# Kernel tuning notes

Hardware: AMD Instinct MI355X
Metric: run time of the kernel (lower is better)

The kernel has to match this reference:

```python
import jax, jax.numpy as jnp
import numpy as np

D_MODEL = 1024
NUM_HEADS = 16
HEAD_DIM = D_MODEL // NUM_HEADS
BATCH = 2
SEQ = 2048


def setup_inputs() -> dict:
    key = jax.random.key(0)
    ks = jax.random.split(key, 9)
    s = 1.0 / np.sqrt(D_MODEL)
    inp = {
        "x": jax.random.normal(ks[0], (BATCH, SEQ, D_MODEL), dtype=jnp.float32),
        "mask": jnp.ones((BATCH, SEQ), dtype=jnp.int32),
        "Wq": jax.random.uniform(ks[1], (D_MODEL, D_MODEL), jnp.float32, -s, s),
        "bq": jax.random.uniform(ks[2], (D_MODEL,), jnp.float32, -s, s),
        "Wk": jax.random.uniform(ks[3], (D_MODEL, D_MODEL), jnp.float32, -s, s),
        "bk": jax.random.uniform(ks[4], (D_MODEL,), jnp.float32, -s, s),
        "Wv": jax.random.uniform(ks[5], (D_MODEL, D_MODEL), jnp.float32, -s, s),
        "bv": jax.random.uniform(ks[6], (D_MODEL,), jnp.float32, -s, s),
        "Wo": jax.random.uniform(ks[7], (D_MODEL, D_MODEL), jnp.float32, -s, s),
        "bo": jax.random.uniform(ks[8], (D_MODEL,), jnp.float32, -s, s),
    }
    return inp


def reference(x, mask, Wq, bq, Wk, bk, Wv, bv, Wo, bo):
    B, S, D = x.shape
    H, Hd = NUM_HEADS, HEAD_DIM
    # torch Linear: y = x @ W.T + b ; then reshape to [B, H, S, Hd]
    def proj(W, b):
        return (x @ W.T + b).reshape(B, S, H, Hd).transpose(0, 2, 1, 3)
    Q = proj(Wq, bq)
    K = proj(Wk, bk)
    V = proj(Wv, bv)
    scale = 1.0 / jnp.sqrt(jnp.asarray(Hd, dtype=x.dtype))
    scores = jnp.einsum("bhqd,bhkd->bhqk", Q, K) * scale  # [B,H,S,S]
    # mask [B,S] -> broadcast over query positions; masked_fill(mask==0, -1e9)
    scores = jnp.where(mask[:, None, None, :] == 0, jnp.asarray(-1e9, x.dtype), scores)
    attn = jax.nn.softmax(scores, axis=-1)
    context = jnp.einsum("bhqk,bhkd->bhqd", attn, V)
    context = context.transpose(0, 2, 1, 3).reshape(B, S, D)
    return context @ Wo.T + bo
```

## Files before the change

### kernel.cpp

```cpp
#include <hip/hip_runtime.h>
#include <hip/hip_bf16.h>
#include <cstdint>

#define D_MODEL 1024
#define NUM_HEADS 16
#define HEAD_DIM 64
#define BATCH 2
#define SEQ 2048
#define MROWS (BATCH * SEQ)

typedef __attribute__((ext_vector_type(8))) short bf16x8;
typedef __attribute__((ext_vector_type(4))) float f32x4;
typedef unsigned short u16;

#define QSCALE (0.125f * 1.44269504f)

#if __has_builtin(__builtin_amdgcn_exp2f)
#define EXP2F(x) __builtin_amdgcn_exp2f(x)
#else
#define EXP2F(x) exp2f(x)
#endif

static __device__ __forceinline__ u16 f2bf(float f) {
    unsigned int u = __float_as_uint(f);
    unsigned int lsb = (u >> 16) & 1u;
    u += 0x7fffu + lsb;
    return (u16)(u >> 16);
}

#if __has_builtin(__builtin_amdgcn_cvt_pk_bf16_f32)
static __device__ __forceinline__ unsigned pkbf(float a, float b) {
    typedef __attribute__((ext_vector_type(2))) __bf16 bf2;
    union { bf2 v; unsigned u; } cv;
    cv.v = __builtin_amdgcn_cvt_pk_bf16_f32(a, b);
    return cv.u;
}
#else
static __device__ __forceinline__ unsigned pkbf(float a, float b) {
    unsigned ua = (__float_as_uint(a) + 0x8000u) >> 16;
    unsigned ub = (__float_as_uint(b) + 0x8000u) & 0xffff0000u;
    return ua | ub;
}
#endif

static __device__ __forceinline__ void gload_lds16(const void* g, void* l) {
    __builtin_amdgcn_global_load_lds((const __attribute__((address_space(1))) unsigned int*)g,
                                     (__attribute__((address_space(3))) unsigned int*)l,
                                     16, 0, 0);
}

__global__ void cvt_all(const float* __restrict__ x,
                        const float* __restrict__ w0, const float* __restrict__ w1,
                        const float* __restrict__ w2, const float* __restrict__ w3,
                        u16* __restrict__ base) {
    const int which = blockIdx.y;
    const int NE = D_MODEL * D_MODEL;
    const float* s;
    if (which < 4)      s = x + (size_t)which * NE;
    else if (which == 4) s = w0;
    else if (which == 5) s = w1;
    else if (which == 6) s = w2;
    else                 s = w3;
    u16* dst = base + (size_t)which * NE;
    const int i = (blockIdx.x * blockDim.x + threadIdx.x) * 4;
    float4 v = *(const float4*)(s + i);
    ushort4 o;
    o.x = f2bf(v.x); o.y = f2bf(v.y); o.z = f2bf(v.z); o.w = f2bf(v.w);
    *(ushort4*)(dst + i) = o;
}

template<int BN, int MODE>
__global__ __launch_bounds__(256, 3)
void gemm_staged(const u16* __restrict__ A, const u16* __restrict__ W,
                 const float* __restrict__ b0, const float* __restrict__ b1,
                 const float* __restrict__ b2,
                 u16* __restrict__ o0, u16* __restrict__ o1, u16* __restrict__ o2,
                 float* __restrict__ of, int K, int N) {
    constexpr int WN = BN / 2;
    constexpr int NJ = WN / 16;
    __shared__ __align__(16) u16 As[128 * 64];
    __shared__ __align__(16) u16 Bs[BN * 64];
    __shared__ __align__(16) u16 T[64 * 136];

    const int lane = threadIdx.x & 63;
    const int w    = threadIdx.x >> 6;
    const int quad = lane >> 4;
    const int l16  = lane & 15;
    const int wm = w >> 1, wn = w & 1;

    const u16* Ablk = A + (size_t)(blockIdx.y * 128) * K;
    const u16* Wblk = W + (size_t)(blockIdx.x * BN) * K;

    const int srow = lane >> 3;
    const int scol = lane & 7;

    f32x4 acc[4][NJ];
#pragma unroll
    for (int i = 0; i < 4; ++i)
#pragma unroll
        for (int j = 0; j < NJ; ++j) acc[i][j] = (f32x4){0.f, 0.f, 0.f, 0.f};

    for (int kb0 = 0; kb0 < K; kb0 += 64) {
        __syncthreads();
#pragma unroll
        for (int t = 0; t < 4; ++t) {
            const int r  = w * 32 + t * 8 + srow;
            const int cg = scol ^ (r & 7);
            gload_lds16(Ablk + (size_t)r * K + kb0 + cg * 8, &As[(w * 32 + t * 8) * 64]);
        }
#pragma unroll
        for (int t = 0; t < BN / 32; ++t) {
            const int r  = w * (BN / 4) + t * 8 + srow;
            const int cg = scol ^ (r & 7);
            gload_lds16(Wblk + (size_t)r * K + kb0 + cg * 8, &Bs[(w * (BN / 4) + t * 8) * 64]);
        }
        __syncthreads();
#pragma unroll
        for (int ks = 0; ks < 2; ++ks) {
            bf16x8 a[4], b[NJ];
#pragma unroll
            for (int i = 0; i < 4; ++i) {
                const int ra = wm * 64 + 16 * i + l16;
                a[i] = *(const bf16x8*)&As[ra * 64 + ((ks * 4 + quad) ^ (ra & 7)) * 8];
            }
#pragma unroll
            for (int j = 0; j < NJ; ++j) {
                const int rb = wn * WN + 16 * j + l16;
                b[j] = *(const bf16x8*)&Bs[rb * 64 + ((ks * 4 + quad) ^ (rb & 7)) * 8];
            }
#pragma unroll
            for (int i = 0; i < 4; ++i)
#pragma unroll
                for (int j = 0; j < NJ; ++j)
                    acc[i][j] = __builtin_amdgcn_mfma_f32_16x16x32_bf16(a[i], b[j], acc[i][j], 0, 0, 0);
        }
    }

    const int mbase = blockIdx.y * 128 + wm * 64;
    const int nbase = blockIdx.x * BN + wn * WN;

    if (MODE == 0 && blockIdx.x >= 16) {
        const int mb    = blockIdx.y * 128;
        const int bb    = mb >> 11;
        const int sbase = mb & 2047;
#pragma unroll
        for (int p = 0; p < 2; ++p) {
            __syncthreads();
            if (wn == p) {
#pragma unroll
                for (int j = 0; j < NJ; ++j) {
                    const int nl = 16 * j + l16;
                    const float bv = b2[(nbase + 16 * j + l16) & 1023];
#pragma unroll
                    for (int i = 0; i < 4; ++i) {
                        const int ml = wm * 64 + 16 * i + quad * 4;
                        uint2 pk;
                        pk.x = pkbf(acc[i][j][0] + bv, acc[i][j][1] + bv);
                        pk.y = pkbf(acc[i][j][2] + bv, acc[i][j][3] + bv);
                        *(uint2*)&T[nl * 136 + ml] = pk;
                    }
                }
            }
            __syncthreads();
            const int row = threadIdx.x >> 2;
            const int gn2 = blockIdx.x * 128 + p * 64 + row;
            const int rem2 = gn2 & 1023;
            const int h = rem2 >> 6, d = rem2 & 63;
            u16* dstrow = o2 + (((size_t)(bb * NUM_HEADS + h) * 64) + d) * SEQ + sbase;
#pragma unroll
            for (int k = 0; k < 4; ++k) {
                const int chunk = (threadIdx.x & 3) * 4 + k;
                *(uint4*)(dstrow + chunk * 8) = *(const uint4*)&T[row * 136 + chunk * 8];
            }
        }
        return;
    }

    if (MODE == 0) {
#pragma unroll
        for (int j = 0; j < NJ; ++j) {
            const int gn = nbase + 16 * j + l16;
            const int which = gn >> 10, rem = gn & 1023;
            const float bv = (which == 0 ? b0 : b1)[rem];
            u16* dst = (which == 0) ? o0 : o1;
            const float scl = (which == 0) ? QSCALE : 1.0f;
            const int h = rem >> 6, d = rem & 63;
#pragma unroll
            for (int i = 0; i < 4; ++i)
#pragma unroll
                for (int r = 0; r < 4; ++r) {
                    const int gm = mbase + 16 * i + quad * 4 + r;
                    const int bb = gm >> 11, s = gm & 2047;
                    dst[(((size_t)(bb * NUM_HEADS + h) * SEQ) + s) * 64 + d] =
                        f2bf((acc[i][j][r] + bv) * scl);
                }
        }
    } else {
#pragma unroll
        for (int j = 0; j < NJ; ++j) {
            const int gn = nbase + 16 * j + l16;
            const float bv = b0[gn];
#pragma unroll
            for (int i = 0; i < 4; ++i)
#pragma unroll
                for (int r = 0; r < 4; ++r) {
                    const int gm = mbase + 16 * i + quad * 4 + r;
                    of[(size_t)gm * N + gn] = acc[i][j][r] + bv;
                }
        }
    }
}

__global__ __launch_bounds__(512, 4)
void attn_kernel(const u16* __restrict__ Q, const u16* __restrict__ K,
                 const u16* __restrict__ VT, const int* __restrict__ mask,
                 u16* __restrict__ ctx) {
    __shared__ __align__(16) u16 Ks[2][64 * 64];
    __shared__ __align__(16) u16 Vs[2][64 * 64];
    __shared__ __align__(16) u16 Ps[8][16 * 64];

    const int lane = threadIdx.x & 63;
    const int w    = threadIdx.x >> 6;
    const int quad = lane >> 4;
    const int l16  = lane & 15;

    const int bh = blockIdx.x & 31;
    const int qb = blockIdx.x >> 5;
    const int b  = bh >> 4;
    const int h  = bh & 15;
    const int qbase = qb * 128 + w * 16;

    const u16* Qh = Q + (size_t)bh * SEQ * 64;
    const u16* Kh = K + (size_t)bh * SEQ * 64;
    const u16* Vh = VT + (size_t)bh * 64 * SEQ;
    const int* mrow = mask + b * SEQ;

    const int srow = lane >> 3;
    const int scol = lane & 7;
    const int cg   = scol ^ srow;

    gload_lds16(Kh + (size_t)(8 * w + srow) * 64 + cg * 8, &Ks[0][(8 * w) * 64]);
    gload_lds16(Vh + (size_t)(8 * w + srow) * SEQ + cg * 8, &Vs[0][(8 * w) * 64]);

    bf16x8 qf[2];
#pragma unroll
    for (int ks = 0; ks < 2; ++ks)
        qf[ks] = *(const bf16x8*)(Qh + (size_t)(qbase + l16) * 64 + 32 * ks + quad * 8);

    unsigned dirty = 0;
#pragma unroll
    for (int i = 0; i < 8; ++i) {
        const int4 m4 = *(const int4*)(mrow + i * 256 + lane * 4);
        const bool ok = (m4.x != 0) & (m4.y != 0) & (m4.z != 0) & (m4.w != 0);
        const unsigned long long bal = __ballot(ok);
#pragma unroll
        for (int g = 0; g < 4; ++g)
            if (((bal >> (16 * g)) & 0xffffull) != 0xffffull) dirty |= 1u << (i * 4 + g);
    }

    f32x4 o[4];
#pragma unroll
    for (int id = 0; id < 4; ++id) o[id] = (f32x4){0.f, 0.f, 0.f, 0.f};
    float lst = 0.f;
    const f32x4 fzero = (f32x4){0.f, 0.f, 0.f, 0.f};

    unsigned short* myp = &Ps[w][0];
    const int rowsel = (lane & 48) | (quad * 4);
    const int e3 = l16 & 7;

#pragma unroll 2
    for (int kb = 0; kb < 32; ++kb) {
        const int cur = kb & 1;
        __syncthreads();

        if (kb != 31) {
            const int kn = (kb + 1) * 64;
            gload_lds16(Kh + (size_t)(kn + 8 * w + srow) * 64 + cg * 8,
                        &Ks[cur ^ 1][(8 * w) * 64]);
            gload_lds16(Vh + (size_t)(8 * w + srow) * SEQ + kn + cg * 8,
                        &Vs[cur ^ 1][(8 * w) * 64]);
        }

        const int kstart = kb * 64;
        const bool clean = ((dirty >> kb) & 1u) == 0u;

        bf16x8 kf[4][2];
#pragma unroll
        for (int ik = 0; ik < 4; ++ik) {
            const int row = 16 * ik + l16;
#pragma unroll
            for (int ks = 0; ks < 2; ++ks)
                kf[ik][ks] = *(const bf16x8*)&Ks[cur][row * 64 + ((4 * ks + quad) ^ (row & 7)) * 8];
        }

        f32x4 s[4];
#pragma unroll
        for (int ik = 0; ik < 4; ++ik) {
            f32x4 t = __builtin_amdgcn_mfma_f32_16x16x32_bf16(kf[ik][0], qf[0], fzero, 0, 0, 0);
            t = __builtin_amdgcn_mfma_f32_16x16x32_bf16(kf[ik][1], qf[1], t, 0, 0, 0);
            s[ik] = t;
        }

        bf16x8 vf[4][2];
#pragma unroll
        for (int id = 0; id < 4; ++id) {
            const int row = 16 * id + l16;
#pragma unroll
            for (int ks = 0; ks < 2; ++ks)
                vf[id][ks] = *(const bf16x8*)&Vs[cur][row * 64 + ((4 * ks + quad) ^ (row & 7)) * 8];
        }

        if (!clean) {
#pragma unroll
            for (int ik = 0; ik < 4; ++ik) {
                int4 mk = *(const int4*)(mrow + kstart + 16 * ik + quad * 4);
                const int* mp = (const int*)&mk;
#pragma unroll
                for (int r = 0; r < 4; ++r)
                    s[ik][r] = (mp[r] != 0) ? s[ik][r] : -1e9f;
            }
        }

        float rs = 0.f;
#pragma unroll
        for (int ik = 0; ik < 4; ++ik) {
            const float p0 = EXP2F(fminf(s[ik][0], 80.f));
            const float p1 = EXP2F(fminf(s[ik][1], 80.f));
            const float p2 = EXP2F(fminf(s[ik][2], 80.f));
            const float p3 = EXP2F(fminf(s[ik][3], 80.f));
            rs += (p0 + p1) + (p2 + p3);
            uint2 pk;
            pk.x = pkbf(p0, p1);
            pk.y = pkbf(p2, p3);
            const int wch = (2 * ik + (quad >> 1)) ^ e3;
            *(uint2*)(myp + l16 * 64 + wch * 8 + (quad & 1) * 4) = pk;
        }
        rs += __shfl_xor(rs, 16, 64);
        rs += __shfl_xor(rs, 32, 64);
        lst += rs;

#pragma unroll
        for (int ks = 0; ks < 2; ++ks) {
            bf16x8 pf = *(const bf16x8*)(myp + l16 * 64 + ((4 * ks + quad) ^ e3) * 8);
#pragma unroll
            for (int id = 0; id < 4; ++id)
                o[id] = __builtin_amdgcn_mfma_f32_16x16x32_bf16(pf, vf[id][ks], o[id], 0, 0, 0);
        }
    }

    float linv[4];
#pragma unroll
    for (int r = 0; r < 4; ++r) linv[r] = 1.f / __shfl(lst, rowsel + r, 64);
#pragma unroll
    for (int id = 0; id < 4; ++id)
#pragma unroll
        for (int r = 0; r < 4; ++r) {
            const int q = qbase + quad * 4 + r;
            const int d = 16 * id + l16;
            ctx[((size_t)(b * SEQ + q)) * D_MODEL + h * 64 + d] = f2bf(o[id][r] * linv[r]);
        }
}

extern "C" void kernel_launch(void* const* d_in, const int* in_sizes, int n_in,
                              void* d_out, int out_size, void* d_ws, size_t ws_size,
                              hipStream_t stream) {
    const float* x    = (const float*)d_in[0];
    const int*   mask = (const int*)d_in[1];
    const float* Wq   = (const float*)d_in[2];
    const float* bq   = (const float*)d_in[3];
    const float* Wk   = (const float*)d_in[4];
    const float* bk   = (const float*)d_in[5];
    const float* Wv   = (const float*)d_in[6];
    const float* bv   = (const float*)d_in[7];
    const float* Wo   = (const float*)d_in[8];
    const float* bo   = (const float*)d_in[9];

    u16* xb  = (u16*)d_ws;
    u16* wqb = xb  + (size_t)MROWS * D_MODEL;
    u16* wob = wqb + (size_t)3 * D_MODEL * D_MODEL;
    u16* Qb  = wob + (size_t)D_MODEL * D_MODEL;
    u16* Kb  = Qb  + (size_t)MROWS * D_MODEL;
    u16* VTb = Kb  + (size_t)MROWS * D_MODEL;
    u16* ctx = VTb + (size_t)MROWS * D_MODEL;

    cvt_all<<<dim3(D_MODEL * D_MODEL / 1024, 8), 256, 0, stream>>>(
        x, Wq, Wk, Wv, Wo, xb);

    gemm_staged<128, 0><<<dim3(3 * D_MODEL / 128, MROWS / 128), 256, 0, stream>>>(
        xb, wqb, bq, bk, bv, Qb, Kb, VTb, nullptr, D_MODEL, 3 * D_MODEL);

    attn_kernel<<<BATCH * NUM_HEADS * (SEQ / 128), 512, 0, stream>>>(Qb, Kb, VTb, mask, ctx);

    gemm_staged<64, 1><<<dim3(D_MODEL / 64, MROWS / 128), 256, 0, stream>>>(
        ctx, wob, bo, nullptr, nullptr, nullptr, nullptr, nullptr,
        (float*)d_out, D_MODEL, D_MODEL);
}
```

Measured before the change: 194.8 us.

## Split attention over key halves with combine kernel and register-resident P via permlane

The attention kernel now splits each (batch, head, query-block) over two halves of the key sequence, doubling grid size to 1024 blocks, and writes unnormalized fp32 partial outputs and row sums to workspace. A new combine kernel adds the two partials, normalizes them and converts the result to bf16 ctx. The P tile is no longer staged through shared memory; it is rearranged in registers with permlane32/16 swaps, and V fragments are loaded just before each MFMA. This targets low occupancy and LDS traffic, at the cost of extra fp32 global writes and reads (about 32MB) plus an additional launch.

```diff
diff --git a/kernel.cpp b/kernel.cpp
--- a/kernel.cpp
+++ b/kernel.cpp
@@ -11,6 +11,7 @@
 
 typedef __attribute__((ext_vector_type(8))) short bf16x8;
 typedef __attribute__((ext_vector_type(4))) float f32x4;
+typedef __attribute__((ext_vector_type(2))) unsigned u32x2;
 typedef unsigned short u16;
 
 #define QSCALE (0.125f * 1.44269504f)
@@ -40,6 +41,35 @@
     unsigned ua = (__float_as_uint(a) + 0x8000u) >> 16;
     unsigned ub = (__float_as_uint(b) + 0x8000u) & 0xffff0000u;
     return ua | ub;
+}
+#endif
+
+#if __has_builtin(__builtin_amdgcn_permlane32_swap)
+static __device__ __forceinline__ void plswap32(unsigned &a, unsigned &b) {
+    u32x2 r = __builtin_amdgcn_permlane32_swap(a, b, false, false);
+    a = r[0]; b = r[1];
+}
+#else
+static __device__ __forceinline__ void plswap32(unsigned &a, unsigned &b) {
+    const bool lo = ((threadIdx.x & 63) < 32);
+    unsigned sa = __shfl_xor((int)a, 32, 64), sb = __shfl_xor((int)b, 32, 64);
+    unsigned na = lo ? a : sb;
+    unsigned nb = lo ? sa : b;
+    a = na; b = nb;
+}
+#endif
+#if __has_builtin(__builtin_amdgcn_permlane16_swap)
+static __device__ __forceinline__ void plswap16(unsigned &a, unsigned &b) {
+    u32x2 r = __builtin_amdgcn_permlane16_swap(a, b, false, false);
+    a = r[0]; b = r[1];
+}
+#else
+static __device__ __forceinline__ void plswap16(unsigned &a, unsigned &b) {
+    const bool ev = (((threadIdx.x & 63) >> 4) & 1) == 0;
+    unsigned sa = __shfl_xor((int)a, 16, 64), sb = __shfl_xor((int)b, 16, 64);
+    unsigned na = ev ? a : sb;
+    unsigned nb = ev ? sa : b;
+    a = na; b = nb;
 }
 #endif
 
@@ -211,28 +241,31 @@
     }
 }
 
-__global__ __launch_bounds__(512, 4)
+#define HTILES 16
+__global__ __launch_bounds__(512, 8)
 void attn_kernel(const u16* __restrict__ Q, const u16* __restrict__ K,
                  const u16* __restrict__ VT, const int* __restrict__ mask,
-                 u16* __restrict__ ctx) {
+                 float* __restrict__ Op, float* __restrict__ Lp) {
     __shared__ __align__(16) u16 Ks[2][64 * 64];
     __shared__ __align__(16) u16 Vs[2][64 * 64];
-    __shared__ __align__(16) u16 Ps[8][16 * 64];
 
     const int lane = threadIdx.x & 63;
     const int w    = threadIdx.x >> 6;
     const int quad = lane >> 4;
     const int l16  = lane & 15;
 
-    const int bh = blockIdx.x & 31;
-    const int qb = blockIdx.x >> 5;
+    const int bh   = blockIdx.x & 31;
+    const int qh   = blockIdx.x >> 5;
+    const int qb   = qh & 15;
+    const int half = qh >> 4;
     const int b  = bh >> 4;
     const int h  = bh & 15;
     const int qbase = qb * 128 + w * 16;
+    const int koff  = half * 1024;
 
     const u16* Qh = Q + (size_t)bh * SEQ * 64;
-    const u16* Kh = K + (size_t)bh * SEQ * 64;
-    const u16* Vh = VT + (size_t)bh * 64 * SEQ;
+    const u16* Kh = K + (size_t)bh * SEQ * 64 + (size_t)koff * 64;
+    const u16* Vh = VT + (size_t)bh * 64 * SEQ + koff;
     const int* mrow = mask + b * SEQ;
 
     const int srow = lane >> 3;
@@ -249,8 +282,8 @@
 
     unsigned dirty = 0;
 #pragma unroll
-    for (int i = 0; i < 8; ++i) {
-        const int4 m4 = *(const int4*)(mrow + i * 256 + lane * 4);
+    for (int i = 0; i < 4; ++i) {
+        const int4 m4 = *(const int4*)(mrow + koff + i * 256 + lane * 4);
         const bool ok = (m4.x != 0) & (m4.y != 0) & (m4.z != 0) & (m4.w != 0);
         const unsigned long long bal = __ballot(ok);
 #pragma unroll
@@ -264,16 +297,12 @@
     float lst = 0.f;
     const f32x4 fzero = (f32x4){0.f, 0.f, 0.f, 0.f};
 
-    unsigned short* myp = &Ps[w][0];
-    const int rowsel = (lane & 48) | (quad * 4);
-    const int e3 = l16 & 7;
-
 #pragma unroll 2
-    for (int kb = 0; kb < 32; ++kb) {
+    for (int kb = 0; kb < HTILES; ++kb) {
         const int cur = kb & 1;
         __syncthreads();
 
-        if (kb != 31) {
+        if (kb != HTILES - 1) {
             const int kn = (kb + 1) * 64;
             gload_lds16(Kh + (size_t)(kn + 8 * w + srow) * 64 + cg * 8,
                         &Ks[cur ^ 1][(8 * w) * 64]);
@@ -301,19 +330,10 @@
             s[ik] = t;
         }
 
-        bf16x8 vf[4][2];
-#pragma unroll
-        for (int id = 0; id < 4; ++id) {
-            const int row = 16 * id + l16;
-#pragma unroll
-            for (int ks = 0; ks < 2; ++ks)
-                vf[id][ks] = *(const bf16x8*)&Vs[cur][row * 64 + ((4 * ks + quad) ^ (row & 7)) * 8];
-        }
-
         if (!clean) {
 #pragma unroll
             for (int ik = 0; ik < 4; ++ik) {
-                int4 mk = *(const int4*)(mrow + kstart + 16 * ik + quad * 4);
+                int4 mk = *(const int4*)(mrow + koff + kstart + 16 * ik + quad * 4);
                 const int* mp = (const int*)&mk;
 #pragma unroll
                 for (int r = 0; r < 4; ++r)
@@ -322,6 +342,7 @@
         }
 
         float rs = 0.f;
+        unsigned c[4][2];
 #pragma unroll
         for (int ik = 0; ik < 4; ++ik) {
             const float p0 = EXP2F(fminf(s[ik][0], 80.f));
@@ -329,36 +350,64 @@
             const float p2 = EXP2F(fminf(s[ik][2], 80.f));
             const float p3 = EXP2F(fminf(s[ik][3], 80.f));
             rs += (p0 + p1) + (p2 + p3);
-            uint2 pk;
-            pk.x = pkbf(p0, p1);
-            pk.y = pkbf(p2, p3);
-            const int wch = (2 * ik + (quad >> 1)) ^ e3;
-            *(uint2*)(myp + l16 * 64 + wch * 8 + (quad & 1) * 4) = pk;
+            c[ik][0] = pkbf(p0, p1);
+            c[ik][1] = pkbf(p2, p3);
         }
         rs += __shfl_xor(rs, 16, 64);
         rs += __shfl_xor(rs, 32, 64);
         lst += rs;
 
+        plswap32(c[0][0], c[1][0]); plswap32(c[0][1], c[1][1]);
+        plswap16(c[0][0], c[1][0]); plswap16(c[0][1], c[1][1]);
+        plswap32(c[2][0], c[3][0]); plswap32(c[2][1], c[3][1]);
+        plswap16(c[2][0], c[3][0]); plswap16(c[2][1], c[3][1]);
+        union U { bf16x8 v; unsigned d[4]; };
+        U u0, u1;
+        u0.d[0] = c[0][0]; u0.d[1] = c[0][1]; u0.d[2] = c[1][0]; u0.d[3] = c[1][1];
+        u1.d[0] = c[2][0]; u1.d[1] = c[2][1]; u1.d[2] = c[3][0]; u1.d[3] = c[3][1];
+
 #pragma unroll
         for (int ks = 0; ks < 2; ++ks) {
-            bf16x8 pf = *(const bf16x8*)(myp + l16 * 64 + ((4 * ks + quad) ^ e3) * 8);
-#pragma unroll
-            for (int id = 0; id < 4; ++id)
-                o[id] = __builtin_amdgcn_mfma_f32_16x16x32_bf16(pf, vf[id][ks], o[id], 0, 0, 0);
+            const bf16x8 pf = (ks == 0) ? u0.v : u1.v;
+#pragma unroll
+            for (int id = 0; id < 4; ++id) {
+                const int row = 16 * id + l16;
+                const bf16x8 vfr = *(const bf16x8*)&Vs[cur][row * 64 + ((4 * ks + quad) ^ (row & 7)) * 8];
+                o[id] = __builtin_amdgcn_mfma_f32_16x16x32_bf16(pf, vfr, o[id], 0, 0, 0);
+            }
         }
     }
 
-    float linv[4];
-#pragma unroll
-    for (int r = 0; r < 4; ++r) linv[r] = 1.f / __shfl(lst, rowsel + r, 64);
+    float* Oh = Op + (size_t)half * MROWS * D_MODEL;
 #pragma unroll
     for (int id = 0; id < 4; ++id)
 #pragma unroll
         for (int r = 0; r < 4; ++r) {
             const int q = qbase + quad * 4 + r;
-            const int d = 16 * id + l16;
-            ctx[((size_t)(b * SEQ + q)) * D_MODEL + h * 64 + d] = f2bf(o[id][r] * linv[r]);
-        }
+            Oh[((size_t)(b * SEQ + q)) * D_MODEL + h * 64 + 16 * id + l16] = o[id][r];
+        }
+    if (quad == 0)
+        Lp[((size_t)half * 32 + bh) * SEQ + qbase + l16] = lst;
+}
+
+__global__ __launch_bounds__(256)
+void combine_kernel(const float* __restrict__ Op, const float* __restrict__ Lp,
+                    u16* __restrict__ ctx) {
+    const int gid = blockIdx.x * 256 + threadIdx.x;
+    const int row = gid >> 8;
+    const int c0  = (gid & 255) * 4;
+    const int b = row >> 11, s = row & 2047, h = c0 >> 6;
+    const float l0 = Lp[((size_t)(b * 16 + h)) * SEQ + s];
+    const float l1 = Lp[((size_t)(32 + b * 16 + h)) * SEQ + s];
+    const float inv = 1.f / (l0 + l1);
+    const float4 a  = *(const float4*)(Op + (size_t)row * D_MODEL + c0);
+    const float4 b4 = *(const float4*)(Op + (size_t)MROWS * D_MODEL + (size_t)row * D_MODEL + c0);
+    ushort4 o;
+    o.x = f2bf((a.x + b4.x) * inv);
+    o.y = f2bf((a.y + b4.y) * inv);
+    o.z = f2bf((a.z + b4.z) * inv);
+    o.w = f2bf((a.w + b4.w) * inv);
+    *(ushort4*)(ctx + (size_t)row * D_MODEL + c0) = o;
 }
 
 extern "C" void kernel_launch(void* const* d_in, const int* in_sizes, int n_in,
@@ -382,6 +431,8 @@
     u16* Kb  = Qb  + (size_t)MROWS * D_MODEL;
     u16* VTb = Kb  + (size_t)MROWS * D_MODEL;
     u16* ctx = VTb + (size_t)MROWS * D_MODEL;
+    float* Op = (float*)(ctx + (size_t)MROWS * D_MODEL);
+    float* Lp = Op + (size_t)2 * MROWS * D_MODEL;
 
     cvt_all<<<dim3(D_MODEL * D_MODEL / 1024, 8), 256, 0, stream>>>(
         x, Wq, Wk, Wv, Wo, xb);
@@ -389,7 +440,10 @@
     gemm_staged<128, 0><<<dim3(3 * D_MODEL / 128, MROWS / 128), 256, 0, stream>>>(
         xb, wqb, bq, bk, bv, Qb, Kb, VTb, nullptr, D_MODEL, 3 * D_MODEL);
 
-    attn_kernel<<<BATCH * NUM_HEADS * (SEQ / 128), 512, 0, stream>>>(Qb, Kb, VTb, mask, ctx);
+    attn_kernel<<<2 * BATCH * NUM_HEADS * (SEQ / 128), 512, 0, stream>>>(
+        Qb, Kb, VTb, mask, Op, Lp);
+
+    combine_kernel<<<MROWS * D_MODEL / (256 * 4), 256, 0, stream>>>(Op, Lp, ctx);
 
     gemm_staged<64, 1><<<dim3(D_MODEL / 64, MROWS / 128), 256, 0, stream>>>(
         ctx, wob, bo, nullptr, nullptr, nullptr, nullptr, nullptr,
```

Result: slower. 216.7 us (+11.2%).

## Reshuffle P in registers via permlane swaps instead of LDS round-trip

Applied to the files above, without the earlier changes.

Replaces the per-wave LDS staging of softmax probabilities with in-register permlane32/permlane16 swaps that rearrange the packed bf16 values into the MFMA A-operand layout. This removes LDS writes and reads plus the related waits, and shrinks shared memory for the attention kernel and for the non-MODE-0 GEMM path. It also drops the fminf clamp before exp2 and adds s_setprio around the MFMA groups. The clamp removal relies on scores never overflowing exp2, which only holds because softmax runs without max subtraction.

```diff
diff --git a/kernel.cpp b/kernel.cpp
--- a/kernel.cpp
+++ b/kernel.cpp
@@ -11,6 +11,7 @@
 
 typedef __attribute__((ext_vector_type(8))) short bf16x8;
 typedef __attribute__((ext_vector_type(4))) float f32x4;
+typedef __attribute__((ext_vector_type(2))) unsigned u32x2;
 typedef unsigned short u16;
 
 #define QSCALE (0.125f * 1.44269504f)
@@ -40,6 +41,35 @@
     unsigned ua = (__float_as_uint(a) + 0x8000u) >> 16;
     unsigned ub = (__float_as_uint(b) + 0x8000u) & 0xffff0000u;
     return ua | ub;
+}
+#endif
+
+#if __has_builtin(__builtin_amdgcn_permlane32_swap)
+static __device__ __forceinline__ void plswap32(unsigned &a, unsigned &b) {
+    u32x2 r = __builtin_amdgcn_permlane32_swap(a, b, false, false);
+    a = r[0]; b = r[1];
+}
+#else
+static __device__ __forceinline__ void plswap32(unsigned &a, unsigned &b) {
+    const bool lo = ((threadIdx.x & 63) < 32);
+    unsigned sa = __shfl_xor((int)a, 32, 64), sb = __shfl_xor((int)b, 32, 64);
+    unsigned na = lo ? a : sb;
+    unsigned nb = lo ? sa : b;
+    a = na; b = nb;
+}
+#endif
+#if __has_builtin(__builtin_amdgcn_permlane16_swap)
+static __device__ __forceinline__ void plswap16(unsigned &a, unsigned &b) {
+    u32x2 r = __builtin_amdgcn_permlane16_swap(a, b, false, false);
+    a = r[0]; b = r[1];
+}
+#else
+static __device__ __forceinline__ void plswap16(unsigned &a, unsigned &b) {
+    const bool ev = (((threadIdx.x & 63) >> 4) & 1) == 0;
+    unsigned sa = __shfl_xor((int)a, 16, 64), sb = __shfl_xor((int)b, 16, 64);
+    unsigned na = ev ? a : sb;
+    unsigned nb = ev ? sa : b;
+    a = na; b = nb;
 }
 #endif
 
@@ -80,7 +110,7 @@
     constexpr int NJ = WN / 16;
     __shared__ __align__(16) u16 As[128 * 64];
     __shared__ __align__(16) u16 Bs[BN * 64];
-    __shared__ __align__(16) u16 T[64 * 136];
+    __shared__ __align__(16) u16 T[(MODE == 0) ? 64 * 136 : 16];
 
     const int lane = threadIdx.x & 63;
     const int w    = threadIdx.x >> 6;
@@ -217,7 +247,6 @@
                  u16* __restrict__ ctx) {
     __shared__ __align__(16) u16 Ks[2][64 * 64];
     __shared__ __align__(16) u16 Vs[2][64 * 64];
-    __shared__ __align__(16) u16 Ps[8][16 * 64];
 
     const int lane = threadIdx.x & 63;
     const int w    = threadIdx.x >> 6;
@@ -263,10 +292,7 @@
     for (int id = 0; id < 4; ++id) o[id] = (f32x4){0.f, 0.f, 0.f, 0.f};
     float lst = 0.f;
     const f32x4 fzero = (f32x4){0.f, 0.f, 0.f, 0.f};
-
-    unsigned short* myp = &Ps[w][0];
     const int rowsel = (lane & 48) | (quad * 4);
-    const int e3 = l16 & 7;
 
 #pragma unroll 2
     for (int kb = 0; kb < 32; ++kb) {
@@ -294,12 +320,14 @@
         }
 
         f32x4 s[4];
+        __builtin_amdgcn_s_setprio(1);
 #pragma unroll
         for (int ik = 0; ik < 4; ++ik) {
             f32x4 t = __builtin_amdgcn_mfma_f32_16x16x32_bf16(kf[ik][0], qf[0], fzero, 0, 0, 0);
             t = __builtin_amdgcn_mfma_f32_16x16x32_bf16(kf[ik][1], qf[1], t, 0, 0, 0);
             s[ik] = t;
         }
+        __builtin_amdgcn_s_setprio(0);
 
         bf16x8 vf[4][2];
 #pragma unroll
@@ -322,30 +350,39 @@
         }
 
         float rs = 0.f;
+        unsigned c[4][2];
 #pragma unroll
         for (int ik = 0; ik < 4; ++ik) {
-            const float p0 = EXP2F(fminf(s[ik][0], 80.f));
-            const float p1 = EXP2F(fminf(s[ik][1], 80.f));
-            const float p2 = EXP2F(fminf(s[ik][2], 80.f));
-            const float p3 = EXP2F(fminf(s[ik][3], 80.f));
+            const float p0 = EXP2F(s[ik][0]);
+            const float p1 = EXP2F(s[ik][1]);
+            const float p2 = EXP2F(s[ik][2]);
+            const float p3 = EXP2F(s[ik][3]);
             rs += (p0 + p1) + (p2 + p3);
-            uint2 pk;
-            pk.x = pkbf(p0, p1);
-            pk.y = pkbf(p2, p3);
-            const int wch = (2 * ik + (quad >> 1)) ^ e3;
-            *(uint2*)(myp + l16 * 64 + wch * 8 + (quad & 1) * 4) = pk;
+            c[ik][0] = pkbf(p0, p1);
+            c[ik][1] = pkbf(p2, p3);
         }
         rs += __shfl_xor(rs, 16, 64);
         rs += __shfl_xor(rs, 32, 64);
         lst += rs;
 
+        plswap32(c[0][0], c[1][0]); plswap32(c[0][1], c[1][1]);
+        plswap16(c[0][0], c[1][0]); plswap16(c[0][1], c[1][1]);
+        plswap32(c[2][0], c[3][0]); plswap32(c[2][1], c[3][1]);
+        plswap16(c[2][0], c[3][0]); plswap16(c[2][1], c[3][1]);
+        union U { bf16x8 v; unsigned d[4]; };
+        U u0, u1;
+        u0.d[0] = c[0][0]; u0.d[1] = c[0][1]; u0.d[2] = c[1][0]; u0.d[3] = c[1][1];
+        u1.d[0] = c[2][0]; u1.d[1] = c[2][1]; u1.d[2] = c[3][0]; u1.d[3] = c[3][1];
+
+        __builtin_amdgcn_s_setprio(1);
 #pragma unroll
         for (int ks = 0; ks < 2; ++ks) {
-            bf16x8 pf = *(const bf16x8*)(myp + l16 * 64 + ((4 * ks + quad) ^ e3) * 8);
+            const bf16x8 pf = (ks == 0) ? u0.v : u1.v;
 #pragma unroll
             for (int id = 0; id < 4; ++id)
                 o[id] = __builtin_amdgcn_mfma_f32_16x16x32_bf16(pf, vf[id][ks], o[id], 0, 0, 0);
         }
+        __builtin_amdgcn_s_setprio(0);
     }
 
     float linv[4];
```

Result: faster. 190.6 us (-2.2%).
